# Optimization experiments

Measured on AMD Instinct MI355X. Metric: run time of the kernel, lower is better.

The kernel has to match this reference:

```python
import jax, jax.numpy as jnp
import numpy as np

NUM_EXPERTS = 8
TOP_K = 2
HIDDEN = 2048
INTER = 1408
NUM_TOKENS = 8192


def setup_inputs() -> dict:
    key = jax.random.key(0)
    k1, k2, k3, k4 = jax.random.split(key, 4)
    hidden_states = jax.random.normal(k1, (NUM_TOKENS, HIDDEN), dtype=jnp.float32)
    router_weight = jax.random.normal(k2, (NUM_EXPERTS, HIDDEN), dtype=jnp.float32) * 0.02
    gate_up_proj = jax.random.normal(k3, (NUM_EXPERTS, 2 * INTER, HIDDEN), dtype=jnp.float32) * 0.02
    down_proj = jax.random.normal(k4, (NUM_EXPERTS, HIDDEN, INTER), dtype=jnp.float32) * 0.02
    return {
        "hidden_states": hidden_states,
        "router_weight": router_weight,
        "gate_up_proj": gate_up_proj,
        "down_proj": down_proj,
    }


def reference(hidden_states, router_weight, gate_up_proj, down_proj):
    T, H = hidden_states.shape
    E = router_weight.shape[0]
    dtype = hidden_states.dtype

    # Router: logits -> fp32 softmax -> top-k -> normalize -> cast back
    logits = hidden_states @ router_weight.T                      # [T, E]
    probs = jax.nn.softmax(logits.astype(jnp.float32), axis=-1)
    rw, sel = jax.lax.top_k(probs, TOP_K)                          # [T, K]
    rw = rw / jnp.sum(rw, axis=-1, keepdims=True)                  # norm_topk_prob=True
    rw = rw.astype(dtype)

    # Dense combine weights per token per expert (zero for unselected experts)
    combine = jnp.zeros((T, E), dtype=dtype)
    combine = combine.at[jnp.arange(T)[:, None], sel].add(rw)      # [T, E]

    out = jnp.zeros_like(hidden_states)
    for e in range(E):  # small fixed loop over experts
        gate_up = hidden_states @ gate_up_proj[e].T                # [T, 2I]
        gate, up = jnp.split(gate_up, 2, axis=-1)
        h = jax.nn.silu(gate) * up                                 # SiluAndMul
        expert_out = h @ down_proj[e].T                            # [T, H]
        out = out + combine[:, e:e + 1] * expert_out
    return out
```

## Files before the change

### kernel.cpp

```cpp
#include <hip/hip_runtime.h>
#include <hip/hip_bf16.h>
#include <stdint.h>
#include <math.h>


#define E_ 8
#define H_ 2048
#define I_ 1408
#define T_ 8192
#define NSLOT (T_ * 2)
#define NBLK 64

typedef __bf16 bf16;
typedef bf16 bf16x4 __attribute__((ext_vector_type(4)));
typedef bf16 bf16x8 __attribute__((ext_vector_type(8)));
typedef float f32x4 __attribute__((ext_vector_type(4)));

__device__ inline void gl2lds16(const void* g, void* l) {
  __builtin_amdgcn_global_load_lds(
      (const __attribute__((address_space(1))) unsigned int*)g,
      (__attribute__((address_space(3))) unsigned int*)l, 16, 0, 0);
}

__global__ __launch_bounds__(256) void cvtw_k(const float* __restrict__ a, int n8a,
                                              const float* __restrict__ b, int n8b,
                                              bf16* __restrict__ oa,
                                              bf16* __restrict__ ob) {
  int stride = gridDim.x * blockDim.x;
  int ntot = n8a + n8b;
  for (int i = blockIdx.x * blockDim.x + threadIdx.x; i < ntot; i += stride) {
    const float* src; bf16* dst; int k;
    if (i < n8a) { src = a; dst = oa; k = i; }
    else         { src = b; dst = ob; k = i - n8a; }
    const float4* p = (const float4*)src + (size_t)k * 2;
    float4 x = p[0], y = p[1];
    bf16x8 o;
    o[0] = (bf16)x.x; o[1] = (bf16)x.y; o[2] = (bf16)x.z; o[3] = (bf16)x.w;
    o[4] = (bf16)y.x; o[5] = (bf16)y.y; o[6] = (bf16)y.z; o[7] = (bf16)y.w;
    *((bf16x8*)dst + k) = o;
  }
}

__global__ __launch_bounds__(256) void router_k(const float* __restrict__ X,
                                                const float* __restrict__ R,
                                                bf16* __restrict__ xbf,
                                                int* __restrict__ sel,
                                                float* __restrict__ wts) {
  int lane = threadIdx.x & 63;
  int t = blockIdx.x * 4 + (threadIdx.x >> 6);
  const float4* x4 = (const float4*)(X + (size_t)t * H_);
  bf16x4* xb4 = (bf16x4*)(xbf + (size_t)t * H_);
  float acc[E_];
#pragma unroll
  for (int e = 0; e < E_; ++e) acc[e] = 0.f;
#pragma unroll
  for (int i = 0; i < H_ / 256; ++i) {
    float4 x = x4[i * 64 + lane];
    bf16x4 xo; xo[0] = (bf16)x.x; xo[1] = (bf16)x.y; xo[2] = (bf16)x.z; xo[3] = (bf16)x.w;
    xb4[i * 64 + lane] = xo;
#pragma unroll
    for (int e = 0; e < E_; ++e) {
      float4 r = ((const float4*)(R + (size_t)e * H_))[i * 64 + lane];
      acc[e] += x.x * r.x + x.y * r.y + x.z * r.z + x.w * r.w;
    }
  }
#pragma unroll
  for (int e = 0; e < E_; ++e)
#pragma unroll
    for (int off = 32; off > 0; off >>= 1) acc[e] += __shfl_xor(acc[e], off);
  if (lane == 0) {
    int e1 = 0; float l1 = acc[0];
#pragma unroll
    for (int e = 1; e < E_; ++e) if (acc[e] > l1) { l1 = acc[e]; e1 = e; }
    int e2 = -1; float l2 = -3.4e38f;
#pragma unroll
    for (int e = 0; e < E_; ++e) if (e != e1 && acc[e] > l2) { l2 = acc[e]; e2 = e; }
    float d = expf(l2 - l1);
    float inv = 1.f / (1.f + d);
    sel[2 * t] = e1; sel[2 * t + 1] = e2;
    wts[2 * t] = inv; wts[2 * t + 1] = d * inv;
  }
}

__global__ __launch_bounds__(256) void count_k(const int* __restrict__ sel,
                                               int* __restrict__ blockHist) {
  __shared__ int h[E_];
  int t = threadIdx.x;
  if (t < E_) h[t] = 0;
  __syncthreads();
  atomicAdd(&h[sel[blockIdx.x * 256 + t]], 1);
  __syncthreads();
  if (t < E_) blockHist[blockIdx.x * E_ + t] = h[t];
}

__global__ __launch_bounds__(64) void plan_k(const int* __restrict__ blockHist,
                                             int* __restrict__ ctl,
                                             int* __restrict__ blockBase) {
  __shared__ int cnts[E_], offs[E_];
  int t = threadIdx.x;
  if (t < E_) {
    int c = 0;
    for (int b = 0; b < NBLK; ++b) c += blockHist[b * E_ + t];
    cnts[t] = c; ctl[t] = c;
  }
  __syncthreads();
  if (t == 0) {
    int off = 0;
    for (int e = 0; e < E_; ++e) { offs[e] = off; ctl[8 + e] = off; off += cnts[e]; }
  }
  __syncthreads();
  if (t < E_) {
    int run = offs[t];
    for (int b = 0; b < NBLK; ++b) {
      blockBase[b * E_ + t] = run;
      run += blockHist[b * E_ + t];
    }
  }
}

__global__ __launch_bounds__(256) void scatter_k(const int* __restrict__ sel,
                                                 const float* __restrict__ wts,
                                                 const int* __restrict__ blockBase,
                                                 int* __restrict__ tok,
                                                 float* __restrict__ sw,
                                                 int* __restrict__ inv) {
  __shared__ int wcnt[4][E_];
  int t = threadIdx.x;
  int lane = t & 63, w = t >> 6;
  int i = blockIdx.x * 256 + t;
  int e = sel[i];
  unsigned long long below = (lane == 63) ? ~0ull >> 1 : (1ull << lane) - 1;
  int myrank = 0;
#pragma unroll
  for (int e0 = 0; e0 < E_; ++e0) {
    unsigned long long m = __ballot(e == e0);
    if (e == e0) myrank = __popcll(m & below);
    if (lane == 0) wcnt[w][e0] = __popcll(m);
  }
  __syncthreads();
  int pos = blockBase[blockIdx.x * E_ + e] + myrank;
#pragma unroll
  for (int w2 = 0; w2 < 3; ++w2)
    if (w2 < w) pos += wcnt[w2][e];
  tok[pos] = i >> 1;
  sw[pos] = wts[i];
  inv[i] = pos;
}

__global__ __launch_bounds__(256) void gemm1_k(const bf16* __restrict__ Xb,
                                               const bf16* __restrict__ Wgu,
                                               const int* __restrict__ ctl,
                                               const int* __restrict__ tok,
                                               bf16* __restrict__ act) {
  constexpr int NJ = I_ / 64;
  constexpr int NM = T_ / 128;
  constexpr int NB = NJ * NM * E_;
  const int L0 = ((int)blockIdx.x & 7) * (NB >> 3) + ((int)blockIdx.x >> 3);
  const int e = L0 / (NJ * NM);
  const int rem = L0 - e * (NJ * NM);
  const int m0 = (rem / NJ) * 128;
  const int j0 = (rem % NJ) * 64;
  const int cnt = ctl[e];
  if (m0 >= cnt) return;
  const int base = ctl[8 + e];

  __shared__ alignas(16) bf16 lA[2][128 * 64];
  __shared__ alignas(16) bf16 lBg[2][64 * 64];
  __shared__ alignas(16) bf16 lBu[2][64 * 64];

  const int t = threadIdx.x;
  const int lane = t & 63;
  const int wr = (t >> 7) & 1;
  const int wc = (t >> 6) & 1;
  const int lo = lane & 15, hi = lane >> 4;
  const bf16* wg = Wgu + (size_t)e * (2 * I_) * H_;

  const bf16* asrc[4]; int aoff[4];
#pragma unroll
  for (int c = 0; c < 4; ++c) {
    int L = c * 256 + t;
    int row = L >> 3, cc = (L & 7) ^ (row & 7);
    int r = m0 + row; if (r >= cnt) r = cnt - 1;
    asrc[c] = Xb + (size_t)tok[base + r] * H_ + cc * 8;
    aoff[c] = L * 16;
  }
  const bf16* gsrc[2]; const bf16* usrc[2]; int boff[2];
#pragma unroll
  for (int c = 0; c < 2; ++c) {
    int L = c * 256 + t;
    int row = L >> 3, cc = (L & 7) ^ (row & 7);
    gsrc[c] = wg + (size_t)(j0 + row) * H_ + cc * 8;
    usrc[c] = wg + (size_t)(I_ + j0 + row) * H_ + cc * 8;
    boff[c] = L * 16;
  }

#define STG1(b, k)                                                \
  {                                                               \
    _Pragma("unroll")                                             \
    for (int c = 0; c < 4; ++c)                                   \
      gl2lds16(asrc[c] + (k), (char*)lA[b] + aoff[c]);            \
    _Pragma("unroll")                                             \
    for (int c = 0; c < 2; ++c) {                                 \
      gl2lds16(gsrc[c] + (k), (char*)lBg[b] + boff[c]);           \
      gl2lds16(usrc[c] + (k), (char*)lBu[b] + boff[c]);           \
    }                                                             \
  }

  f32x4 zero = {0.f, 0.f, 0.f, 0.f};
  f32x4 ag[4][2], au[4][2];
#pragma unroll
  for (int m = 0; m < 4; ++m)
#pragma unroll
    for (int n = 0; n < 2; ++n) { ag[m][n] = zero; au[m][n] = zero; }

  STG1(0, 0);
  __syncthreads();

  for (int k0 = 0; k0 < H_; k0 += 128) {
#pragma unroll
    for (int p = 0; p < 2; ++p) {
      const int kc = k0 + p * 64;
      if (kc + 64 < H_) STG1(p ^ 1, kc + 64);
#pragma unroll
      for (int kk = 0; kk < 2; ++kk) {
        const int chunk = kk * 4 + hi;
        bf16x8 af[4], bg[2], bu[2];
#pragma unroll
        for (int m = 0; m < 4; ++m) {
          int row = wr * 64 + m * 16 + lo;
          af[m] = *(const bf16x8*)((const char*)lA[p] + row * 128 + ((chunk ^ (row & 7)) * 16));
        }
#pragma unroll
        for (int n = 0; n < 2; ++n) {
          int row = wc * 32 + n * 16 + lo;
          int sw2 = (chunk ^ (row & 7)) * 16;
          bg[n] = *(const bf16x8*)((const char*)lBg[p] + row * 128 + sw2);
          bu[n] = *(const bf16x8*)((const char*)lBu[p] + row * 128 + sw2);
        }
#pragma unroll
        for (int m = 0; m < 4; ++m)
#pragma unroll
          for (int n = 0; n < 2; ++n) {
            ag[m][n] = __builtin_amdgcn_mfma_f32_16x16x32_bf16(af[m], bg[n], ag[m][n], 0, 0, 0);
            au[m][n] = __builtin_amdgcn_mfma_f32_16x16x32_bf16(af[m], bu[n], au[m][n], 0, 0, 0);
          }
      }
      __syncthreads();
    }
  }
#undef STG1

#pragma unroll
  for (int m = 0; m < 4; ++m)
#pragma unroll
    for (int r = 0; r < 4; ++r) {
      int row = m0 + wr * 64 + m * 16 + hi * 4 + r;
      if (row < cnt) {
        bf16* dst = act + (size_t)(base + row) * I_ + j0 + wc * 32 + lo;
#pragma unroll
        for (int n = 0; n < 2; ++n) {
          float g = ag[m][n][r], u = au[m][n][r];
          dst[n * 16] = (bf16)(g / (1.f + __expf(-g)) * u);
        }
      }
    }
}

__global__ __launch_bounds__(256) void gemm2_k(const bf16* __restrict__ act,
                                               const bf16* __restrict__ Wd,
                                               const int* __restrict__ ctl,
                                               const float* __restrict__ sw,
                                               bf16* __restrict__ y) {
  constexpr int NJ = H_ / 128;
  constexpr int NM = T_ / 128;
  constexpr int NB = NJ * NM * E_;
  const int L0 = ((int)blockIdx.x & 7) * (NB >> 3) + ((int)blockIdx.x >> 3);
  const int e = L0 / (NJ * NM);
  const int rem = L0 - e * (NJ * NM);
  const int m0 = (rem / NJ) * 128;
  const int n0 = (rem % NJ) * 128;
  const int cnt = ctl[e];
  if (m0 >= cnt) return;
  const int base = ctl[8 + e];

  __shared__ alignas(16) bf16 lA[2][128 * 64];
  __shared__ alignas(16) bf16 lB[2][128 * 64];

  const int t = threadIdx.x;
  const int lane = t & 63;
  const int wr = (t >> 7) & 1;
  const int wc = (t >> 6) & 1;
  const int lo = lane & 15, hi = lane >> 4;
  const bf16* wd = Wd + (size_t)e * H_ * I_;

  const bf16* asrc[4]; int aoff[4];
#pragma unroll
  for (int c = 0; c < 4; ++c) {
    int L = c * 256 + t;
    int row = L >> 3, cc = (L & 7) ^ (row & 7);
    int r = m0 + row; if (r >= cnt) r = cnt - 1;
    asrc[c] = act + (size_t)(base + r) * I_ + cc * 8;
    aoff[c] = L * 16;
  }
  const bf16* bsrc[4]; int boff[4];
#pragma unroll
  for (int c = 0; c < 4; ++c) {
    int L = c * 256 + t;
    int row = L >> 3, cc = (L & 7) ^ (row & 7);
    bsrc[c] = wd + (size_t)(n0 + row) * I_ + cc * 8;
    boff[c] = L * 16;
  }

#define STG2(b, k)                                                \
  {                                                               \
    _Pragma("unroll")                                             \
    for (int c = 0; c < 4; ++c)                                   \
      gl2lds16(asrc[c] + (k), (char*)lA[b] + aoff[c]);            \
    _Pragma("unroll")                                             \
    for (int c = 0; c < 4; ++c)                                   \
      gl2lds16(bsrc[c] + (k), (char*)lB[b] + boff[c]);            \
  }

  f32x4 zero = {0.f, 0.f, 0.f, 0.f};
  f32x4 acc[4][4];
#pragma unroll
  for (int m = 0; m < 4; ++m)
#pragma unroll
    for (int n = 0; n < 4; ++n) acc[m][n] = zero;

  STG2(0, 0);
  __syncthreads();

  for (int k0 = 0; k0 < I_; k0 += 128) {
#pragma unroll
    for (int p = 0; p < 2; ++p) {
      const int kc = k0 + p * 64;
      if (kc + 64 < I_) STG2(p ^ 1, kc + 64);
#pragma unroll
      for (int kk = 0; kk < 2; ++kk) {
        const int chunk = kk * 4 + hi;
        bf16x8 af[4], bb[4];
#pragma unroll
        for (int m = 0; m < 4; ++m) {
          int row = wr * 64 + m * 16 + lo;
          af[m] = *(const bf16x8*)((const char*)lA[p] + row * 128 + ((chunk ^ (row & 7)) * 16));
        }
#pragma unroll
        for (int n = 0; n < 4; ++n) {
          int row = wc * 64 + n * 16 + lo;
          bb[n] = *(const bf16x8*)((const char*)lB[p] + row * 128 + ((chunk ^ (row & 7)) * 16));
        }
#pragma unroll
        for (int m = 0; m < 4; ++m)
#pragma unroll
          for (int n = 0; n < 4; ++n)
            acc[m][n] = __builtin_amdgcn_mfma_f32_16x16x32_bf16(af[m], bb[n], acc[m][n], 0, 0, 0);
      }
      __syncthreads();
    }
  }
#undef STG2

#pragma unroll
  for (int m = 0; m < 4; ++m)
#pragma unroll
    for (int r = 0; r < 4; ++r) {
      int row = m0 + wr * 64 + m * 16 + hi * 4 + r;
      if (row < cnt) {
        float w = sw[base + row];
        bf16* dst = y + (size_t)(base + row) * H_ + n0 + wc * 64 + lo;
#pragma unroll
        for (int n = 0; n < 4; ++n) dst[n * 16] = (bf16)(w * acc[m][n][r]);
      }
    }
}

__global__ __launch_bounds__(256) void combine_k(const bf16* __restrict__ y,
                                                 const int* __restrict__ inv,
                                                 float* __restrict__ out) {
  int idx = blockIdx.x * 256 + threadIdx.x;
  int t = idx >> 8;
  int c = idx & 255;
  int i1 = inv[2 * t], i2 = inv[2 * t + 1];
  bf16x8 a = *((const bf16x8*)(y + (size_t)i1 * H_) + c);
  bf16x8 b = *((const bf16x8*)(y + (size_t)i2 * H_) + c);
  float* op = out + (size_t)t * H_ + c * 8;
#pragma unroll
  for (int k = 0; k < 8; ++k) op[k] = (float)a[k] + (float)b[k];
}

extern "C" void kernel_launch(void* const* d_in, const int* in_sizes, int n_in,
                              void* d_out, int out_size, void* d_ws, size_t ws_size,
                              hipStream_t stream) {
  const float* X = (const float*)d_in[0];
  const float* R = (const float*)d_in[1];
  const float* Wgu = (const float*)d_in[2];
  const float* Wd = (const float*)d_in[3];
  float* out = (float*)d_out;

  char* ws = (char*)d_ws;
  size_t o = 0;
  auto alloc = [&](size_t sz) { void* p = ws + o; o += (sz + 255) & ~(size_t)255; return p; };
  bf16* wgu_bf = (bf16*)alloc(sizeof(bf16) * (size_t)E_ * 2 * I_ * H_);
  bf16* wd_bf  = (bf16*)alloc(sizeof(bf16) * (size_t)E_ * H_ * I_);
  bf16* xbf    = (bf16*)alloc(sizeof(bf16) * (size_t)T_ * H_);
  bf16* actb   = (bf16*)alloc(sizeof(bf16) * (size_t)NSLOT * I_);
  int* sel     = (int*)alloc(4 * NSLOT);
  float* wts   = (float*)alloc(4 * NSLOT);
  int* tokb    = (int*)alloc(4 * NSLOT);
  float* swb   = (float*)alloc(4 * NSLOT);
  int* invb    = (int*)alloc(4 * NSLOT);
  int* ctl     = (int*)alloc(4 * 32);
  int* bh      = (int*)alloc(4 * NBLK * E_);
  int* bb      = (int*)alloc(4 * NBLK * E_);
  bf16* yb = wgu_bf;

  cvtw_k<<<2048, 256, 0, stream>>>(Wgu, (int)((size_t)E_ * 2 * I_ * H_ / 8),
                                   Wd, (int)((size_t)E_ * H_ * I_ / 8),
                                   wgu_bf, wd_bf);
  router_k<<<T_ / 4, 256, 0, stream>>>(X, R, xbf, sel, wts);
  count_k<<<NBLK, 256, 0, stream>>>(sel, bh);
  plan_k<<<1, 64, 0, stream>>>(bh, ctl, bb);
  scatter_k<<<NBLK, 256, 0, stream>>>(sel, wts, bb, tokb, swb, invb);
  gemm1_k<<<(I_ / 64) * (T_ / 128) * E_, 256, 0, stream>>>(xbf, wgu_bf, ctl, tokb, actb);
  gemm2_k<<<(H_ / 128) * (T_ / 128) * E_, 256, 0, stream>>>(actb, wd_bf, ctl, swb, yb);
  combine_k<<<T_ * H_ / 2048, 256, 0, stream>>>(yb, invb, out);
}
```

Baseline: 519.3 us.

## Overlap down-proj weight conversion with gemm1 using idle early-exit blocks

The fp32-to-bf16 conversion of the down-projection weights moves out of the standalone conversion kernel and into gemm1. gemm1 blocks whose row tile exceeds the expert's token count used to exit at once; they now pull chunks from an atomic counter and convert Wd, so that conversion overlaps the grouped GEMM instead of running serially. Both GEMM kernels also get a launch_bounds minimum of 2 blocks per CU. This adds a memset and atomic traffic, and assumes enough idle blocks exist to finish all chunks. Correctness does not depend on that, because the counter loop always completes every chunk before gemm1 ends.

```diff
diff --git a/kernel.cpp b/kernel.cpp
--- a/kernel.cpp
+++ b/kernel.cpp
@@ -10,6 +10,7 @@
 #define T_ 8192
 #define NSLOT (T_ * 2)
 #define NBLK 64
+#define NCHUNK 2816
 
 typedef __bf16 bf16;
 typedef bf16 bf16x4 __attribute__((ext_vector_type(4)));
@@ -22,22 +23,16 @@
       (__attribute__((address_space(3))) unsigned int*)l, 16, 0, 0);
 }
 
-__global__ __launch_bounds__(256) void cvtw_k(const float* __restrict__ a, int n8a,
-                                              const float* __restrict__ b, int n8b,
-                                              bf16* __restrict__ oa,
-                                              bf16* __restrict__ ob) {
+__global__ __launch_bounds__(256) void cvt_k(const float* __restrict__ in,
+                                             bf16* __restrict__ out, int n8) {
   int stride = gridDim.x * blockDim.x;
-  int ntot = n8a + n8b;
-  for (int i = blockIdx.x * blockDim.x + threadIdx.x; i < ntot; i += stride) {
-    const float* src; bf16* dst; int k;
-    if (i < n8a) { src = a; dst = oa; k = i; }
-    else         { src = b; dst = ob; k = i - n8a; }
-    const float4* p = (const float4*)src + (size_t)k * 2;
-    float4 x = p[0], y = p[1];
+  for (int i = blockIdx.x * blockDim.x + threadIdx.x; i < n8; i += stride) {
+    const float4* p = (const float4*)in + (size_t)i * 2;
+    float4 a = p[0], b = p[1];
     bf16x8 o;
-    o[0] = (bf16)x.x; o[1] = (bf16)x.y; o[2] = (bf16)x.z; o[3] = (bf16)x.w;
-    o[4] = (bf16)y.x; o[5] = (bf16)y.y; o[6] = (bf16)y.z; o[7] = (bf16)y.w;
-    *((bf16x8*)dst + k) = o;
+    o[0] = (bf16)a.x; o[1] = (bf16)a.y; o[2] = (bf16)a.z; o[3] = (bf16)a.w;
+    o[4] = (bf16)b.x; o[5] = (bf16)b.y; o[6] = (bf16)b.z; o[7] = (bf16)b.w;
+    *((bf16x8*)out + i) = o;
   }
 }
 
@@ -147,11 +142,14 @@
   inv[i] = pos;
 }
 
-__global__ __launch_bounds__(256) void gemm1_k(const bf16* __restrict__ Xb,
-                                               const bf16* __restrict__ Wgu,
-                                               const int* __restrict__ ctl,
-                                               const int* __restrict__ tok,
-                                               bf16* __restrict__ act) {
+__global__ __launch_bounds__(256, 2) void gemm1_k(const bf16* __restrict__ Xb,
+                                                  const bf16* __restrict__ Wgu,
+                                                  const int* __restrict__ ctl,
+                                                  const int* __restrict__ tok,
+                                                  bf16* __restrict__ act,
+                                                  const float* __restrict__ Wd32,
+                                                  bf16* __restrict__ wdbf,
+                                                  int* __restrict__ cvtc) {
   constexpr int NJ = I_ / 64;
   constexpr int NM = T_ / 128;
   constexpr int NB = NJ * NM * E_;
@@ -161,14 +159,34 @@
   const int m0 = (rem / NJ) * 128;
   const int j0 = (rem % NJ) * 64;
   const int cnt = ctl[e];
-  if (m0 >= cnt) return;
+  const int t = threadIdx.x;
+
+  if (m0 >= cnt) {
+    __shared__ int sc;
+    for (;;) {
+      if (t == 0) sc = atomicAdd(cvtc, 1);
+      __syncthreads();
+      int c = sc;
+      __syncthreads();
+      if (c >= NCHUNK) return;
+#pragma unroll
+      for (int k = 0; k < 4; ++k) {
+        size_t v = (size_t)c * 1024 + k * 256 + t;
+        const float4* p = (const float4*)Wd32 + v * 2;
+        float4 x = p[0], y = p[1];
+        bf16x8 o;
+        o[0] = (bf16)x.x; o[1] = (bf16)x.y; o[2] = (bf16)x.z; o[3] = (bf16)x.w;
+        o[4] = (bf16)y.x; o[5] = (bf16)y.y; o[6] = (bf16)y.z; o[7] = (bf16)y.w;
+        *((bf16x8*)wdbf + v) = o;
+      }
+    }
+  }
   const int base = ctl[8 + e];
 
   __shared__ alignas(16) bf16 lA[2][128 * 64];
   __shared__ alignas(16) bf16 lBg[2][64 * 64];
   __shared__ alignas(16) bf16 lBu[2][64 * 64];
 
-  const int t = threadIdx.x;
   const int lane = t & 63;
   const int wr = (t >> 7) & 1;
   const int wc = (t >> 6) & 1;
@@ -266,11 +284,11 @@
     }
 }
 
-__global__ __launch_bounds__(256) void gemm2_k(const bf16* __restrict__ act,
-                                               const bf16* __restrict__ Wd,
-                                               const int* __restrict__ ctl,
-                                               const float* __restrict__ sw,
-                                               bf16* __restrict__ y) {
+__global__ __launch_bounds__(256, 2) void gemm2_k(const bf16* __restrict__ act,
+                                                  const bf16* __restrict__ Wd,
+                                                  const int* __restrict__ ctl,
+                                                  const float* __restrict__ sw,
+                                                  bf16* __restrict__ y) {
   constexpr int NJ = H_ / 128;
   constexpr int NM = T_ / 128;
   constexpr int NB = NJ * NM * E_;
@@ -413,16 +431,18 @@
   int* ctl     = (int*)alloc(4 * 32);
   int* bh      = (int*)alloc(4 * NBLK * E_);
   int* bb      = (int*)alloc(4 * NBLK * E_);
+  int* cvtc    = (int*)alloc(4 * 64);
   bf16* yb = wgu_bf;
 
-  cvtw_k<<<2048, 256, 0, stream>>>(Wgu, (int)((size_t)E_ * 2 * I_ * H_ / 8),
-                                   Wd, (int)((size_t)E_ * H_ * I_ / 8),
-                                   wgu_bf, wd_bf);
+  hipMemsetAsync(cvtc, 0, 4, stream);
+
+  cvt_k<<<2048, 256, 0, stream>>>(Wgu, wgu_bf, (int)((size_t)E_ * 2 * I_ * H_ / 8));
   router_k<<<T_ / 4, 256, 0, stream>>>(X, R, xbf, sel, wts);
   count_k<<<NBLK, 256, 0, stream>>>(sel, bh);
   plan_k<<<1, 64, 0, stream>>>(bh, ctl, bb);
   scatter_k<<<NBLK, 256, 0, stream>>>(sel, wts, bb, tokb, swb, invb);
-  gemm1_k<<<(I_ / 64) * (T_ / 128) * E_, 256, 0, stream>>>(xbf, wgu_bf, ctl, tokb, actb);
+  gemm1_k<<<(I_ / 64) * (T_ / 128) * E_, 256, 0, stream>>>(xbf, wgu_bf, ctl, tokb,
+                                                           actb, Wd, wd_bf, cvtc);
   gemm2_k<<<(H_ / 128) * (T_ / 128) * E_, 256, 0, stream>>>(actb, wd_bf, ctl, swb, yb);
   combine_k<<<T_ * H_ / 2048, 256, 0, stream>>>(yb, invb, out);
 }
```

New measurement: 586.4 us. 12.9% more time.
